# Optimization experiments

Hardware: AMD Instinct MI355X
Metric: run time of the kernel (lower is better)

Reference implementation:

```python
import jax, jax.numpy as jnp
import numpy as np

N, E = 100000, 1600000
IN_DIM, HID_DIM, OUT_DIM = 128, 64, 32


def setup_inputs() -> dict:
    key = jax.random.key(0)
    k1, k2, k3, k4 = jax.random.split(key, 4)
    x = jax.random.normal(k1, (N, IN_DIM), dtype=jnp.float32)
    edge_index = jax.random.randint(k2, (2, E), 0, N, dtype=jnp.int64)
    # GCNConv weights (glorot) and zero biases, matching PyG defaults
    s1 = float(np.sqrt(6.0 / (IN_DIM + HID_DIM)))
    s2 = float(np.sqrt(6.0 / (HID_DIM + OUT_DIM)))
    W1 = jax.random.uniform(k3, (IN_DIM, HID_DIM), jnp.float32, -s1, s1)
    W2 = jax.random.uniform(k4, (HID_DIM, OUT_DIM), jnp.float32, -s2, s2)
    b1 = jnp.zeros((HID_DIM,), jnp.float32)
    b2 = jnp.zeros((OUT_DIM,), jnp.float32)
    return {"x": x, "W1": W1, "b1": b1, "W2": W2, "b2": b2, "edge_index": edge_index}


def _gcn_conv(x, W, b, row, col, n):
    # x: [N, Fin] -> [N, Fout].  row/col already include self-loops.
    xw = x @ W  # [N, Fout]
    deg = jax.ops.segment_sum(jnp.ones_like(col, dtype=xw.dtype), col, num_segments=n)
    dinv = jnp.where(deg > 0, jax.lax.rsqrt(deg), jnp.zeros_like(deg))
    norm = dinv[row] * dinv[col]  # [E+N]
    out = jax.ops.segment_sum(norm[:, None] * xw[row], col, num_segments=n)
    return out + b


def reference(x, W1, b1, W2, b2, edge_index):
    n = x.shape[0]
    loops = jnp.arange(n, dtype=edge_index.dtype)
    row = jnp.concatenate([edge_index[0], loops])
    col = jnp.concatenate([edge_index[1], loops])
    h = jax.nn.relu(_gcn_conv(x, W1, b1, row, col, n))
    # F.dropout with training=False is the identity (eval-mode reference)
    out = jax.nn.relu(_gcn_conv(h, W2, b2, row, col, n))
    return out
```

## Files before the change

kernel.cpp:

```cpp
#include <hip/hip_runtime.h>

#define IN_DIM  128
#define HID_DIM 64
#define OUT_DIM 32
#define BPN   256
#define CHUNK 4096

typedef __attribute__((ext_vector_type(8))) short bf16x8;
typedef __attribute__((ext_vector_type(4))) float f32x4;

__device__ __forceinline__ unsigned pack_bf16(float a, float b) {
  unsigned ua = __float_as_uint(a), ub = __float_as_uint(b);
  ua += 0x7FFFu + ((ua >> 16) & 1u);
  ub += 0x7FFFu + ((ub >> 16) & 1u);
  return (ua >> 16) | (ub & 0xFFFF0000u);
}
__device__ __forceinline__ float bf_lo(unsigned v) { return __uint_as_float(v << 16); }
__device__ __forceinline__ float bf_hi(unsigned v) { return __uint_as_float(v & 0xFFFF0000u); }

__device__ __forceinline__ int load_idx(const void* p, long long i, int is64) {
  return is64 ? (int)((const long long*)p)[i] : ((const int*)p)[i];
}

__device__ __forceinline__ int block_detect(const void* eidx, long long E,
                                            long long N, int* sflag) {
  bool ok = true;
  long long cap = E < 64 ? E : 64;
  if (threadIdx.x < cap)
    ok = ((const unsigned long long*)eidx)[threadIdx.x] < (unsigned long long)N;
  unsigned long long ball = __ballot(ok);
  if (threadIdx.x == 0) *sflag = (ball == ~0ULL) ? 1 : 0;
  __syncthreads();
  return *sflag;
}

__global__ __launch_bounds__(256) void k_p1(const void* eidx, long long E,
                                            int* __restrict__ binCnt,
                                            long long N, int nbin) {
  __shared__ int hist[4 * 512];
  __shared__ int sflag;
  for (int i = threadIdx.x; i < 4 * 512; i += 256) hist[i] = 0;
  int f = block_detect(eidx, E, N, &sflag);
  int* h = hist + 512 * (threadIdx.x >> 6);
  long long b0 = (long long)blockIdx.x * CHUNK;
#pragma unroll
  for (int i = 0; i < CHUNK / 256; ++i) {
    long long e = b0 + i * 256 + threadIdx.x;
    if (e < E) atomicAdd(&h[load_idx(eidx, E + e, f) >> 8], 1);
  }
  __syncthreads();
  for (int i = threadIdx.x; i < nbin; i += 256) {
    int s = hist[i] + hist[512 + i] + hist[1024 + i] + hist[1536 + i];
    if (s) atomicAdd(&binCnt[i], s);
  }
}

__global__ __launch_bounds__(512) void k_scanbins(const int* __restrict__ binCnt,
                                                  int* __restrict__ binBase,
                                                  int* __restrict__ binCursor, int nbin,
                                                  const float* __restrict__ W1,
                                                  unsigned short* __restrict__ w1t,
                                                  unsigned* __restrict__ xw1b,
                                                  unsigned* __restrict__ xw2b, int N) {
  __shared__ int s[512];
  int t = threadIdx.x;
  if (t < HID_DIM / 2) xw1b[(size_t)N * (HID_DIM / 2) + t] = 0;
  else if (t < HID_DIM / 2 + OUT_DIM / 2)
    xw2b[(size_t)N * (OUT_DIM / 2) + (t - HID_DIM / 2)] = 0;
  for (int i = t; i < HID_DIM * IN_DIM; i += 512) {
    int j = i >> 7, k = i & 127;
    w1t[i] = (unsigned short)(pack_bf16(W1[k * HID_DIM + j], 0.f) & 0xFFFFu);
  }
  int own = (t < nbin) ? binCnt[t] : 0;
  s[t] = own; __syncthreads();
  for (int o = 1; o < 512; o <<= 1) {
    int v = (t >= o) ? s[t - o] : 0;
    __syncthreads();
    s[t] += v;
    __syncthreads();
  }
  if (t < nbin) { int ex = s[t] - own; binBase[t] = ex; binCursor[t] = ex; }
}

__global__ __launch_bounds__(256) void k_p2(const void* eidx, long long E,
                                            int* __restrict__ binCursor,
                                            unsigned* __restrict__ entry1,
                                            long long N, int nbin) {
  __shared__ int hist[512];
  __shared__ int basel[512];
  __shared__ int sflag;
  for (int i = threadIdx.x; i < nbin; i += 256) hist[i] = 0;
  int f = block_detect(eidx, E, N, &sflag);
  long long b0 = (long long)blockIdx.x * CHUNK;
#pragma unroll
  for (int i = 0; i < CHUNK / 256; ++i) {
    long long e = b0 + i * 256 + threadIdx.x;
    if (e < E) atomicAdd(&hist[load_idx(eidx, E + e, f) >> 8], 1);
  }
  __syncthreads();
  for (int i = threadIdx.x; i < nbin; i += 256) {
    int h = hist[i];
    basel[i] = h ? atomicAdd(&binCursor[i], h) : 0;
  }
  __syncthreads();
  for (int i = threadIdx.x; i < nbin; i += 256) hist[i] = 0;
  __syncthreads();
#pragma unroll
  for (int i = 0; i < CHUNK / 256; ++i) {
    long long e = b0 + i * 256 + threadIdx.x;
    if (e < E) {
      int r = load_idx(eidx, e, f);
      int c = load_idx(eidx, E + e, f);
      int bin = c >> 8;
      int rk = atomicAdd(&hist[bin], 1);
      entry1[basel[bin] + rk] = ((unsigned)(c & 255) << 17) | (unsigned)r;
    }
  }
}

__global__ __launch_bounds__(256) void k_p3(const unsigned* __restrict__ entry1,
                                            const int* __restrict__ binBase,
                                            const int* __restrict__ binCnt,
                                            int* __restrict__ entry2,
                                            int* __restrict__ base,
                                            int* __restrict__ cnt,
                                            float* __restrict__ dinv, int N) {
  __shared__ int hist[BPN];
  __shared__ int off[BPN];
  __shared__ int s[BPN];
  int t = threadIdx.x;
  int b = blockIdx.x;
  int lo = binBase[b];
  int hi = lo + binCnt[b];
  int pBB = ((lo + 7) & ~7) + 8 * BPN * b;
  int n0 = b * BPN;
  hist[t] = 0;
  __syncthreads();
  for (int i = lo + t; i < hi; i += 256)
    atomicAdd(&hist[entry1[i] >> 17], 1);
  __syncthreads();
  int own  = hist[t];
  int own8 = (own + 7) & ~7;
  s[t] = own8; __syncthreads();
  for (int o = 1; o < 256; o <<= 1) {
    int v = (t >= o) ? s[t - o] : 0;
    __syncthreads();
    s[t] += v;
    __syncthreads();
  }
  int node = n0 + t;
  int ex = pBB + (s[t] - own8);
  if (node < N) {
    base[node] = ex;
    cnt[node]  = own;
    dinv[node] = rsqrtf((float)own + 1.0f);
    for (int q = own; q < own8; ++q) entry2[ex + q] = N;
  }
  off[t] = ex;
  __syncthreads();
  for (int i = lo + t; i < hi; i += 256) {
    unsigned v = entry1[i];
    int pos = atomicAdd(&off[v >> 17], 1);
    entry2[pos] = (int)(v & 0x1FFFFu);
  }
}

__global__ __launch_bounds__(256) void k_gemm1(const float* __restrict__ x,
                                               const unsigned short* __restrict__ w1t,
                                               const float* __restrict__ dinv,
                                               unsigned* __restrict__ xw1b, int N) {
  __shared__ unsigned short xs[64 * IN_DIM];
  __shared__ unsigned short wt[64 * IN_DIM];
  const int rbase = blockIdx.x * 64;

  {
    const float4* xg = (const float4*)x;
#pragma unroll
    for (int j = 0; j < 8; ++j) {
      int fIdx = threadIdx.x + 256 * j;
      int r = fIdx >> 5, c4 = fIdx & 31;
      int rr = rbase + r; if (rr >= N) rr = N - 1;
      float4 v = xg[(size_t)rr * 32 + c4];
      uint2 pv = make_uint2(pack_bf16(v.x, v.y), pack_bf16(v.z, v.w));
      int chunk = (c4 >> 1) ^ (r & 7);
      *(uint2*)((char*)xs + r * 256 + chunk * 16 + (c4 & 1) * 8) = pv;
    }
  }
  {
    const uint2* wg = (const uint2*)w1t;
#pragma unroll
    for (int j = 0; j < 8; ++j) {
      int fIdx = threadIdx.x + 256 * j;
      int r = fIdx >> 5, q = fIdx & 31;
      uint2 v = wg[fIdx];
      int chunk = (q >> 1) ^ (r & 7);
      *(uint2*)((char*)wt + r * 256 + chunk * 16 + (q & 1) * 8) = v;
    }
  }
  __syncthreads();

  const int wv = threadIdx.x >> 6;
  const int l  = threadIdx.x & 63;
  const int lo16 = l & 15;
  const int hi4  = l >> 4;

  bf16x8 a[4];
#pragma unroll
  for (int ks = 0; ks < 4; ++ks) {
    int row = wv * 16 + lo16;
    int chunk = (ks * 4 + hi4) ^ (row & 7);
    a[ks] = *(const bf16x8*)((const char*)xs + row * 256 + chunk * 16);
  }

  f32x4 acc[4];
#pragma unroll
  for (int ct = 0; ct < 4; ++ct) {
    f32x4 c = {0.f, 0.f, 0.f, 0.f};
#pragma unroll
    for (int ks = 0; ks < 4; ++ks) {
      int col = ct * 16 + lo16;
      int chunk = (ks * 4 + hi4) ^ (col & 7);
      bf16x8 b = *(const bf16x8*)((const char*)wt + col * 256 + chunk * 16);
      c = __builtin_amdgcn_mfma_f32_16x16x32_bf16(a[ks], b, c, 0, 0, 0);
    }
    acc[ct] = c;
  }

  float dvr[4];
#pragma unroll
  for (int i = 0; i < 4; ++i) {
    int row = rbase + wv * 16 + hi4 * 4 + i;
    dvr[i] = (row < N) ? dinv[row] : 0.f;
  }
#pragma unroll
  for (int ct = 0; ct < 4; ++ct) {
#pragma unroll
    for (int i = 0; i < 4; ++i) {
      float v = dvr[i] * acc[ct][i];
      float vp = __shfl_xor(v, 1);
      int row = rbase + wv * 16 + hi4 * 4 + i;
      if ((l & 1) == 0 && row < N) {
        int j = ct * 16 + lo16;
        xw1b[(size_t)row * (HID_DIM / 2) + (j >> 1)] = pack_bf16(v, vp);
      }
    }
  }
}

__global__ __launch_bounds__(256) void k_gather1(const int* __restrict__ entry,
                                                 const int* __restrict__ base,
                                                 const int* __restrict__ cnt,
                                                 const float* __restrict__ dinv,
                                                 const uint2* __restrict__ xw1b2,
                                                 const float* __restrict__ b1,
                                                 const float* __restrict__ W2,
                                                 unsigned* __restrict__ xw2b, int N) {
  __shared__ float w2s[HID_DIM * OUT_DIM];
  __shared__ float hs[16][68];
  __shared__ float dvs[16];
  for (int i = threadIdx.x; i < HID_DIM * OUT_DIM; i += 256) w2s[i] = W2[i];
  __syncthreads();

  const int wv   = threadIdx.x >> 6;
  const int ln   = threadIdx.x & 63;
  const int slot = wv * 4 + (ln >> 4);
  const int lane = ln & 15;
  const int node = blockIdx.x * 16 + slot;

  if (node < N) {
    int st = base[node];
    int it = (cnt[node] + 7) >> 3;
    float ax[4], ay[4], az[4], aw[4];
#pragma unroll
    for (int q = 0; q < 4; ++q) { ax[q] = ay[q] = az[q] = aw[q] = 0.f; }
    for (int i = 0; i < it; ++i) {
      int4 ea = *(const int4*)(entry + st + 8 * i);
      int4 eb = *(const int4*)(entry + st + 8 * i + 4);
      uint2 v0 = xw1b2[(size_t)ea.x * 16 + lane];
      uint2 v1 = xw1b2[(size_t)ea.y * 16 + lane];
      uint2 v2 = xw1b2[(size_t)ea.z * 16 + lane];
      uint2 v3 = xw1b2[(size_t)ea.w * 16 + lane];
      uint2 v4 = xw1b2[(size_t)eb.x * 16 + lane];
      uint2 v5 = xw1b2[(size_t)eb.y * 16 + lane];
      uint2 v6 = xw1b2[(size_t)eb.z * 16 + lane];
      uint2 v7 = xw1b2[(size_t)eb.w * 16 + lane];
      ax[0] += bf_lo(v0.x) + bf_lo(v4.x); ay[0] += bf_hi(v0.x) + bf_hi(v4.x);
      az[0] += bf_lo(v0.y) + bf_lo(v4.y); aw[0] += bf_hi(v0.y) + bf_hi(v4.y);
      ax[1] += bf_lo(v1.x) + bf_lo(v5.x); ay[1] += bf_hi(v1.x) + bf_hi(v5.x);
      az[1] += bf_lo(v1.y) + bf_lo(v5.y); aw[1] += bf_hi(v1.y) + bf_hi(v5.y);
      ax[2] += bf_lo(v2.x) + bf_lo(v6.x); ay[2] += bf_hi(v2.x) + bf_hi(v6.x);
      az[2] += bf_lo(v2.y) + bf_lo(v6.y); aw[2] += bf_hi(v2.y) + bf_hi(v6.y);
      ax[3] += bf_lo(v3.x) + bf_lo(v7.x); ay[3] += bf_hi(v3.x) + bf_hi(v7.x);
      az[3] += bf_lo(v3.y) + bf_lo(v7.y); aw[3] += bf_hi(v3.y) + bf_hi(v7.y);
    }
    uint2 vs = xw1b2[(size_t)node * 16 + lane];
    float dv = dinv[node];
    float4 bb = *(const float4*)(b1 + 4 * lane);
    float h0 = dv * ((ax[0] + ax[1]) + (ax[2] + ax[3]) + bf_lo(vs.x)) + bb.x;
    float h1 = dv * ((ay[0] + ay[1]) + (ay[2] + ay[3]) + bf_hi(vs.x)) + bb.y;
    float h2 = dv * ((az[0] + az[1]) + (az[2] + az[3]) + bf_lo(vs.y)) + bb.z;
    float h3 = dv * ((aw[0] + aw[1]) + (aw[2] + aw[3]) + bf_hi(vs.y)) + bb.w;
    float4 hv;
    hv.x = h0 > 0.f ? h0 : 0.f;
    hv.y = h1 > 0.f ? h1 : 0.f;
    hv.z = h2 > 0.f ? h2 : 0.f;
    hv.w = h3 > 0.f ? h3 : 0.f;
    *(float4*)(&hs[slot][4 * lane]) = hv;
    if (lane == 0) dvs[slot] = dv;
  }
  __builtin_amdgcn_wave_barrier();

  if (node < N) {
    float acc0 = 0.f, acc1 = 0.f;
#pragma unroll
    for (int jj = 0; jj < HID_DIM; ++jj) {
      float hv = hs[slot][jj];
      float2 w = *(const float2*)(w2s + jj * OUT_DIM + 2 * lane);
      acc0 += hv * w.x;
      acc1 += hv * w.y;
    }
    float dv = dvs[slot];
    xw2b[(size_t)node * (OUT_DIM / 2) + lane] = pack_bf16(dv * acc0, dv * acc1);
  }
}

__global__ __launch_bounds__(256) void k_gather2(const int* __restrict__ entry,
                                                 const int* __restrict__ base,
                                                 const int* __restrict__ cnt,
                                                 const float* __restrict__ dinv,
                                                 const uint2* __restrict__ xw2b2,
                                                 const float* __restrict__ b2,
                                                 float* __restrict__ out, int N) {
  const int nl   = threadIdx.x >> 3;
  const int lane = threadIdx.x & 7;
  const int node = blockIdx.x * 32 + nl;
  if (node >= N) return;
  int st = base[node];
  int it = (cnt[node] + 7) >> 3;
  float ax[4], ay[4], az[4], aw[4];
#pragma unroll
  for (int q = 0; q < 4; ++q) { ax[q] = ay[q] = az[q] = aw[q] = 0.f; }
  for (int i = 0; i < it; ++i) {
    int4 ea = *(const int4*)(entry + st + 8 * i);
    int4 eb = *(const int4*)(entry + st + 8 * i + 4);
    uint2 v0 = xw2b2[(size_t)ea.x * 8 + lane];
    uint2 v1 = xw2b2[(size_t)ea.y * 8 + lane];
    uint2 v2 = xw2b2[(size_t)ea.z * 8 + lane];
    uint2 v3 = xw2b2[(size_t)ea.w * 8 + lane];
    uint2 v4 = xw2b2[(size_t)eb.x * 8 + lane];
    uint2 v5 = xw2b2[(size_t)eb.y * 8 + lane];
    uint2 v6 = xw2b2[(size_t)eb.z * 8 + lane];
    uint2 v7 = xw2b2[(size_t)eb.w * 8 + lane];
    ax[0] += bf_lo(v0.x) + bf_lo(v4.x); ay[0] += bf_hi(v0.x) + bf_hi(v4.x);
    az[0] += bf_lo(v0.y) + bf_lo(v4.y); aw[0] += bf_hi(v0.y) + bf_hi(v4.y);
    ax[1] += bf_lo(v1.x) + bf_lo(v5.x); ay[1] += bf_hi(v1.x) + bf_hi(v5.x);
    az[1] += bf_lo(v1.y) + bf_lo(v5.y); aw[1] += bf_hi(v1.y) + bf_hi(v5.y);
    ax[2] += bf_lo(v2.x) + bf_lo(v6.x); ay[2] += bf_hi(v2.x) + bf_hi(v6.x);
    az[2] += bf_lo(v2.y) + bf_lo(v6.y); aw[2] += bf_hi(v2.y) + bf_hi(v6.y);
    ax[3] += bf_lo(v3.x) + bf_lo(v7.x); ay[3] += bf_hi(v3.x) + bf_hi(v7.x);
    az[3] += bf_lo(v3.y) + bf_lo(v7.y); aw[3] += bf_hi(v3.y) + bf_hi(v7.y);
  }
  uint2 vs = xw2b2[(size_t)node * 8 + lane];
  float dv = dinv[node];
  float4 bb = *(const float4*)(b2 + 4 * lane);
  float v0 = dv * ((ax[0] + ax[1]) + (ax[2] + ax[3]) + bf_lo(vs.x)) + bb.x;
  float v1 = dv * ((ay[0] + ay[1]) + (ay[2] + ay[3]) + bf_hi(vs.x)) + bb.y;
  float v2 = dv * ((az[0] + az[1]) + (az[2] + az[3]) + bf_lo(vs.y)) + bb.z;
  float v3 = dv * ((aw[0] + aw[1]) + (aw[2] + aw[3]) + bf_hi(vs.y)) + bb.w;
  float4 res;
  res.x = v0 > 0.f ? v0 : 0.f;
  res.y = v1 > 0.f ? v1 : 0.f;
  res.z = v2 > 0.f ? v2 : 0.f;
  res.w = v3 > 0.f ? v3 : 0.f;
  *(float4*)(out + (size_t)node * OUT_DIM + 4 * lane) = res;
}

static inline size_t align256(size_t x) { return (x + 255) & ~(size_t)255; }

extern "C" void kernel_launch(void* const* d_in, const int* in_sizes, int n_in,
                              void* d_out, int out_size, void* d_ws, size_t ws_size,
                              hipStream_t stream) {
  const float* x   = (const float*)d_in[0];
  const float* W1  = (const float*)d_in[1];
  const float* b1  = (const float*)d_in[2];
  const float* W2  = (const float*)d_in[3];
  const float* b2  = (const float*)d_in[4];
  const void*  eidx = d_in[5];

  const int  N = in_sizes[0] / IN_DIM;
  const long long E = (long long)in_sizes[5] / 2;
  const int  nbin = (N + BPN - 1) / BPN;
  const int  np   = (int)((E + CHUNK - 1) / CHUNK);
  const size_t e2cap = (size_t)E + (size_t)8 * BPN * nbin + 64;

  char* ws = (char*)d_ws;
  size_t off = 0;
  int*      cnt       = (int*)(ws + off);      off += align256((size_t)N * 4);
  float*    dinv      = (float*)(ws + off);    off += align256((size_t)N * 4);
  int*      base      = (int*)(ws + off);      off += align256((size_t)N * 4);
  int*      binCnt    = (int*)(ws + off);      off += align256(512 * 4);
  int*      binBase   = (int*)(ws + off);      off += align256(512 * 4);
  int*      binCursor = (int*)(ws + off);      off += align256(512 * 4);
  unsigned short* w1t = (unsigned short*)(ws + off); off += align256((size_t)HID_DIM * IN_DIM * 2);
  unsigned* entry1    = (unsigned*)(ws + off); off += align256((size_t)E * 4);
  int*      entry2    = (int*)(ws + off);      off += align256(e2cap * 4);
  unsigned* xw1b      = (unsigned*)(ws + off); off += align256((size_t)(N + 1) * (HID_DIM / 2) * 4);
  unsigned* xw2b      = (unsigned*)(ws + off); off += align256((size_t)(N + 1) * (OUT_DIM / 2) * 4);
  float*    outf      = (float*)d_out;

  hipMemsetAsync(binCnt, 0, 512 * 4, stream);

  k_p1<<<np, 256, 0, stream>>>(eidx, E, binCnt, (long long)N, nbin);
  k_scanbins<<<1, 512, 0, stream>>>(binCnt, binBase, binCursor, nbin, W1, w1t, xw1b, xw2b, N);
  k_p2<<<np, 256, 0, stream>>>(eidx, E, binCursor, entry1, (long long)N, nbin);
  k_p3<<<nbin, 256, 0, stream>>>(entry1, binBase, binCnt, entry2, base, cnt, dinv, N);

  k_gemm1<<<(N + 63) / 64, 256, 0, stream>>>(x, w1t, dinv, xw1b, N);

  k_gather1<<<(N + 15) / 16, 256, 0, stream>>>(entry2, base, cnt, dinv,
                                               (const uint2*)xw1b, b1, W2, xw2b, N);

  k_gather2<<<(N + 31) / 32, 256, 0, stream>>>(entry2, base, cnt, dinv,
                                               (const uint2*)xw2b, b2, outf, N);
}
```

Measured before the change: 140.8 us.

## Sort nodes by in-degree to balance gather work across wavefront slots

Builds a degree histogram in k_p3 and a new k_perm kernel that counting-sorts nodes by in-degree (capped at 63) into a permutation. Both gather kernels then process nodes in permuted order, so nodes sharing a wavefront have similar loop trip counts and lanes diverge less. A small kernel replaces the memset to zero the bin and degree counters. This adds an extra kernel launch, an indirection load per node, and scattered output writes, which cost locality.

```diff
diff --git a/kernel.cpp b/kernel.cpp
--- a/kernel.cpp
+++ b/kernel.cpp
@@ -32,6 +32,14 @@
   if (threadIdx.x == 0) *sflag = (ball == ~0ULL) ? 1 : 0;
   __syncthreads();
   return *sflag;
+}
+
+__global__ __launch_bounds__(512) void k_zero(int* __restrict__ binCnt,
+                                              int* __restrict__ degHist,
+                                              int* __restrict__ degCursor) {
+  int t = threadIdx.x;
+  binCnt[t] = 0;
+  if (t < 64) { degHist[t] = 0; degCursor[t] = 0; }
 }
 
 __global__ __launch_bounds__(256) void k_p1(const void* eidx, long long E,
@@ -124,10 +132,12 @@
                                             int* __restrict__ entry2,
                                             int* __restrict__ base,
                                             int* __restrict__ cnt,
-                                            float* __restrict__ dinv, int N) {
+                                            float* __restrict__ dinv,
+                                            int* __restrict__ degHist, int N) {
   __shared__ int hist[BPN];
   __shared__ int off[BPN];
   __shared__ int s[BPN];
+  __shared__ int degh[64];
   int t = threadIdx.x;
   int b = blockIdx.x;
   int lo = binBase[b];
@@ -135,6 +145,7 @@
   int pBB = ((lo + 7) & ~7) + 8 * BPN * b;
   int n0 = b * BPN;
   hist[t] = 0;
+  if (t < 64) degh[t] = 0;
   __syncthreads();
   for (int i = lo + t; i < hi; i += 256)
     atomicAdd(&hist[entry1[i] >> 17], 1);
@@ -154,6 +165,7 @@
     base[node] = ex;
     cnt[node]  = own;
     dinv[node] = rsqrtf((float)own + 1.0f);
+    atomicAdd(&degh[own < 63 ? own : 63], 1);
     for (int q = own; q < own8; ++q) entry2[ex + q] = N;
   }
   off[t] = ex;
@@ -163,6 +175,34 @@
     int pos = atomicAdd(&off[v >> 17], 1);
     entry2[pos] = (int)(v & 0x1FFFFu);
   }
+  __syncthreads();
+  if (t < 64 && degh[t]) atomicAdd(&degHist[t], degh[t]);
+}
+
+__global__ __launch_bounds__(256) void k_perm(const int* __restrict__ cnt,
+                                              const int* __restrict__ degHist,
+                                              int* __restrict__ degCursor,
+                                              int* __restrict__ perm, int N) {
+  __shared__ int dbase[64];
+  __shared__ int lh[64];
+  __shared__ int lb[64];
+  int t = threadIdx.x;
+  if (t < 64) lh[t] = 0;
+  if (t == 0) {
+    int acc = 0;
+    for (int i = 0; i < 64; ++i) { dbase[i] = acc; acc += degHist[i]; }
+  }
+  __syncthreads();
+  int node = blockIdx.x * 256 + t;
+  int d = 0, rk = 0;
+  if (node < N) {
+    d = cnt[node]; if (d > 63) d = 63;
+    rk = atomicAdd(&lh[d], 1);
+  }
+  __syncthreads();
+  if (t < 64) lb[t] = lh[t] ? atomicAdd(&degCursor[t], lh[t]) : 0;
+  __syncthreads();
+  if (node < N) perm[dbase[d] + lb[d] + rk] = node;
 }
 
 __global__ __launch_bounds__(256) void k_gemm1(const float* __restrict__ x,
@@ -247,7 +287,8 @@
   }
 }
 
-__global__ __launch_bounds__(256) void k_gather1(const int* __restrict__ entry,
+__global__ __launch_bounds__(256) void k_gather1(const int* __restrict__ perm,
+                                                 const int* __restrict__ entry,
                                                  const int* __restrict__ base,
                                                  const int* __restrict__ cnt,
                                                  const float* __restrict__ dinv,
@@ -265,9 +306,10 @@
   const int ln   = threadIdx.x & 63;
   const int slot = wv * 4 + (ln >> 4);
   const int lane = ln & 15;
-  const int node = blockIdx.x * 16 + slot;
-
-  if (node < N) {
+  const int sidx = blockIdx.x * 16 + slot;
+  const int node = (sidx < N) ? perm[sidx] : -1;
+
+  if (node >= 0) {
     int st = base[node];
     int it = (cnt[node] + 7) >> 3;
     float ax[4], ay[4], az[4], aw[4];
@@ -310,7 +352,7 @@
   }
   __builtin_amdgcn_wave_barrier();
 
-  if (node < N) {
+  if (node >= 0) {
     float acc0 = 0.f, acc1 = 0.f;
 #pragma unroll
     for (int jj = 0; jj < HID_DIM; ++jj) {
@@ -324,7 +366,8 @@
   }
 }
 
-__global__ __launch_bounds__(256) void k_gather2(const int* __restrict__ entry,
+__global__ __launch_bounds__(256) void k_gather2(const int* __restrict__ perm,
+                                                 const int* __restrict__ entry,
                                                  const int* __restrict__ base,
                                                  const int* __restrict__ cnt,
                                                  const float* __restrict__ dinv,
@@ -333,8 +376,9 @@
                                                  float* __restrict__ out, int N) {
   const int nl   = threadIdx.x >> 3;
   const int lane = threadIdx.x & 7;
-  const int node = blockIdx.x * 32 + nl;
-  if (node >= N) return;
+  const int sidx = blockIdx.x * 32 + nl;
+  if (sidx >= N) return;
+  const int node = perm[sidx];
   int st = base[node];
   int it = (cnt[node] + 7) >> 3;
   float ax[4], ay[4], az[4], aw[4];
@@ -398,9 +442,12 @@
   int*      cnt       = (int*)(ws + off);      off += align256((size_t)N * 4);
   float*    dinv      = (float*)(ws + off);    off += align256((size_t)N * 4);
   int*      base      = (int*)(ws + off);      off += align256((size_t)N * 4);
+  int*      perm      = (int*)(ws + off);      off += align256((size_t)N * 4);
   int*      binCnt    = (int*)(ws + off);      off += align256(512 * 4);
   int*      binBase   = (int*)(ws + off);      off += align256(512 * 4);
   int*      binCursor = (int*)(ws + off);      off += align256(512 * 4);
+  int*      degHist   = (int*)(ws + off);      off += align256(64 * 4);
+  int*      degCursor = (int*)(ws + off);      off += align256(64 * 4);
   unsigned short* w1t = (unsigned short*)(ws + off); off += align256((size_t)HID_DIM * IN_DIM * 2);
   unsigned* entry1    = (unsigned*)(ws + off); off += align256((size_t)E * 4);
   int*      entry2    = (int*)(ws + off);      off += align256(e2cap * 4);
@@ -408,18 +455,19 @@
   unsigned* xw2b      = (unsigned*)(ws + off); off += align256((size_t)(N + 1) * (OUT_DIM / 2) * 4);
   float*    outf      = (float*)d_out;
 
-  hipMemsetAsync(binCnt, 0, 512 * 4, stream);
+  k_zero<<<1, 512, 0, stream>>>(binCnt, degHist, degCursor);
 
   k_p1<<<np, 256, 0, stream>>>(eidx, E, binCnt, (long long)N, nbin);
   k_scanbins<<<1, 512, 0, stream>>>(binCnt, binBase, binCursor, nbin, W1, w1t, xw1b, xw2b, N);
   k_p2<<<np, 256, 0, stream>>>(eidx, E, binCursor, entry1, (long long)N, nbin);
-  k_p3<<<nbin, 256, 0, stream>>>(entry1, binBase, binCnt, entry2, base, cnt, dinv, N);
+  k_p3<<<nbin, 256, 0, stream>>>(entry1, binBase, binCnt, entry2, base, cnt, dinv, degHist, N);
+  k_perm<<<nbin, 256, 0, stream>>>(cnt, degHist, degCursor, perm, N);
 
   k_gemm1<<<(N + 63) / 64, 256, 0, stream>>>(x, w1t, dinv, xw1b, N);
 
-  k_gather1<<<(N + 15) / 16, 256, 0, stream>>>(entry2, base, cnt, dinv,
+  k_gather1<<<(N + 15) / 16, 256, 0, stream>>>(perm, entry2, base, cnt, dinv,
                                                (const uint2*)xw1b, b1, W2, xw2b, N);
 
-  k_gather2<<<(N + 31) / 32, 256, 0, stream>>>(entry2, base, cnt, dinv,
+  k_gather2<<<(N + 31) / 32, 256, 0, stream>>>(perm, entry2, base, cnt, dinv,
                                                (const uint2*)xw2b, b2, outf, N);
 }
```

After: 154.6 us. 9.8% more time.
